# Optimization experiments

Hardware: AMD Instinct MI355X
Metric: run time of the kernel (lower is better)

Reference implementation:

```python
import jax, jax.numpy as jnp
import numpy as np
from jax.scipy.special import logsumexp

B, S, V, H, T = 64, 2048, 32000, 128, 4


def setup_inputs() -> dict:
    key = jax.random.key(0)
    ks = jax.random.split(key, 14)
    s = 0.02
    inp = {
        'x': jax.random.randint(ks[0], (B, S), 1, V),          # token ids (avoid pad idx 0)
        'y': jax.random.randint(ks[1], (B, S), 0, T),           # gold tags
        'mask': jnp.ones((B, S), dtype=bool),
        'emb': (jax.random.normal(ks[2], (V, H)) * s).at[0].set(0.0),  # padding_idx=0
        'w1': jax.random.normal(ks[3], (H, H, 3)) * 0.05,  # OIH conv kernels
        'b1': jnp.zeros((H,)),
        'w2': jax.random.normal(ks[4], (H, H, 3)) * 0.05,
        'b2': jnp.zeros((H,)),
        'w3': jax.random.normal(ks[5], (H, H, 3)) * 0.05,
        'b3': jnp.zeros((H,)),
        'dw': jax.random.normal(ks[6], (H, T)) * s,
        'db': jnp.zeros((T,)),
        'start_t': jax.random.normal(ks[7], (T,)) * 0.1,
        'end_t': jax.random.normal(ks[8], (T,)) * 0.1,
        'trans': jax.random.normal(ks[9], (T, T)) * 0.1,
    }
    return inp


def _conv_relu(h, w, b):
    # h: [B, C, S]; replicate (edge) padding of 1 on sequence axis, kernel 3, stride 1
    hp = jnp.pad(h, ((0, 0), (0, 0), (1, 1)), mode='edge')
    o = jax.lax.conv_general_dilated(hp, w, (1,), 'VALID',
                                     dimension_numbers=('NCH', 'OIH', 'NCH'))
    return jax.nn.relu(o + b[None, :, None])


def _crf_llh(emissions, tags, mask, start_t, end_t, trans):
    # emissions: [B,S,T], tags: [B,S] int, mask: [B,S] bool. torchcrf sum log-likelihood.
    maskf = mask.astype(emissions.dtype)
    bidx = jnp.arange(emissions.shape[0])
    # numerator: score of gold path
    emit = jnp.take_along_axis(emissions, tags[..., None], axis=2)[..., 0]  # [B,S]
    num = start_t[tags[:, 0]] + emit[:, 0]
    tr = trans[tags[:, :-1], tags[:, 1:]]                                    # [B,S-1]
    num = num + ((tr + emit[:, 1:]) * maskf[:, 1:]).sum(axis=1)
    lengths = maskf.sum(axis=1).astype(jnp.int32)
    num = num + end_t[tags[bidx, lengths - 1]]
    # denominator: forward algorithm (sequential logsumexp DP over tags)
    alpha0 = start_t[None, :] + emissions[:, 0]                               # [B,T]
    def step(alpha, xs):
        e_t, m_t = xs                                                         # [B,T], [B]
        nxt = logsumexp(alpha[:, :, None] + trans[None], axis=1) + e_t
        return jnp.where(m_t[:, None], nxt, alpha), None
    alpha, _ = jax.lax.scan(step, alpha0,
                            (emissions[:, 1:].transpose(1, 0, 2), mask[:, 1:].T))
    den = logsumexp(alpha + end_t[None, :], axis=1)                           # [B]
    return (num - den).sum()


def reference(x, y, mask, emb, w1, b1, w2, b2, w3, b3, dw, db, start_t, end_t, trans):
    h = emb[x]                           # [B,S,H]
    h = h.transpose(0, 2, 1)             # [B,H,S] for conv channels
    h = _conv_relu(h, w1, b1)
    h = _conv_relu(h, w2, b2)
    h = _conv_relu(h, w3, b3)
    h = h.transpose(0, 2, 1)             # [B,S,H]
    emissions = jnp.einsum('bsh,ht->bst', h, dw) + db
    return _crf_llh(emissions, y, mask, start_t, end_t, trans)
```

## Files before the change

### kernel.cpp

```cpp
#include <hip/hip_runtime.h>

#define BB 64
#define SS 2048
#define VV 32000
#define HH 128
#define TT 4
#define NSLOT 96
#define CHST (NSLOT*16)
#define BUFSZ (8*CHST)
#define SCL 0x7F7F7F7F

typedef long long i64;
using f32x16 = __attribute__((ext_vector_type(16))) float;
using i32x8  = __attribute__((ext_vector_type(8))) int;

typedef const __attribute__((address_space(1))) unsigned int* gas_ptr;
typedef __attribute__((address_space(3))) unsigned int* las_ptr;

__device__ __forceinline__ unsigned pk4_fp8(float a, float b, float c, float d) {
  unsigned r = __builtin_amdgcn_cvt_pk_fp8_f32(a, b, 0, false);
  r = __builtin_amdgcn_cvt_pk_fp8_f32(c, d, r, true);
  return r;
}
__device__ __forceinline__ unsigned char f2fp8(float v) {
  return (unsigned char)(__builtin_amdgcn_cvt_pk_fp8_f32(v, 0.f, 0, false) & 0xff);
}

__device__ __forceinline__ i32x8 load_af(const char* base) {
  union { i32x8 v; uint4 q[2]; } u;
  u.q[0] = *reinterpret_cast<const uint4*>(base);
  u.q[1] = *reinterpret_cast<const uint4*>(base + CHST);
  return u.v;
}

__global__ __launch_bounds__(256) void pack_kernel(
    const float* __restrict__ w1, const float* __restrict__ w2,
    const float* __restrict__ w3, const float* __restrict__ dw,
    const float* __restrict__ emb,
    unsigned char* __restrict__ wQ8, unsigned char* __restrict__ dwMF,
    unsigned char* __restrict__ emb8)
{
  int idx = blockIdx.x * 256 + threadIdx.x;
  if (idx < 147456) {
    int f = idx >> 11;
    int r = idx & 2047;
    int lane = r >> 5, q = r & 31;
    int kb = f % 6;
    int t2 = f / 6;
    int oq = t2 & 3, layer = t2 >> 2;
    int o = oq * 32 + (lane & 31);
    int k = kb * 64 + (lane >> 5) * 32 + q;
    int tap = k >> 7, i = k & 127;
    const float* w = layer == 0 ? w1 : (layer == 1 ? w2 : w3);
    wQ8[idx] = f2fp8(w[(o * HH + i) * 3 + tap] * 16.f);
  } else if (idx < 151552) {
    int idx2 = idx - 147456;
    int kb = idx2 >> 9;
    int r = idx2 & 511;
    int lane = r >> 3, j = r & 7;
    int row = lane & 31;
    int ch = kb * 16 + (lane >> 5) * 8 + j;
    dwMF[idx2] = (row < 4) ? f2fp8(dw[ch * TT + row] * 16.f) : 0;
  } else {
    int e = idx - 151552;
    if (e < VV * HH / 8) {
      const float* src = emb + (size_t)e * 8;
      float4 f0 = *reinterpret_cast<const float4*>(src);
      float4 f1 = *reinterpret_cast<const float4*>(src + 4);
      uint2 v;
      v.x = pk4_fp8(f0.x * 16.f, f0.y * 16.f, f0.z * 16.f, f0.w * 16.f);
      v.y = pk4_fp8(f1.x * 16.f, f1.y * 16.f, f1.z * 16.f, f1.w * 16.f);
      *reinterpret_cast<uint2*>(emb8 + (size_t)e * 8) = v;
    }
  }
}

__global__ __launch_bounds__(256, 3) void conv_fused(
    const unsigned char* __restrict__ emb8, const int* __restrict__ x,
    const unsigned char* __restrict__ wQ8,
    const float* __restrict__ b1, const float* __restrict__ b2,
    const float* __restrict__ b3,
    const unsigned char* __restrict__ dwMF, const float* __restrict__ db,
    float* __restrict__ emis)
{
  __shared__ char smem[BUFSZ];

  const int blk  = blockIdx.x;
  const int bb   = blk >> 5;
  const int p0   = (blk & 31) << 6;
  const int tid  = threadIdx.x;
  const int lane = tid & 63;
  const int wv   = tid >> 6;
  const int l31  = lane & 31;
  const int lh   = lane >> 5;
  const int oq   = wv;
  const int lhc  = lh * 2 * CHST;

  int swA[3][3], swC[2][3];
#pragma unroll
  for (int pf = 0; pf < 3; pf++)
#pragma unroll
    for (int tap = 0; tap < 3; tap++) {
      int pos = p0 - 16 + pf * 32 + l31 + tap - 1;
      pos = pos < 0 ? 0 : (pos > SS - 1 ? SS - 1 : pos);
      int r = pos - p0 + 16;
      r = r < 0 ? 0 : (r > NSLOT - 1 ? NSLOT - 1 : r);
      swA[pf][tap] = r * 16;
    }
#pragma unroll
  for (int pf = 0; pf < 2; pf++)
#pragma unroll
    for (int tap = 0; tap < 3; tap++) {
      int pos = p0 + pf * 32 + l31 + tap - 1;
      pos = pos < 0 ? 0 : (pos > SS - 1 ? SS - 1 : pos);
      int r = pos - p0 + 16;
      r = r < 0 ? 0 : (r > NSLOT - 1 ? NSLOT - 1 : r);
      swC[pf][tap] = r * 16;
    }

  const unsigned char* wq0 = wQ8 + (size_t)oq * 12288;

  i32x8 wfa = *reinterpret_cast<const i32x8*>(wq0 + lane * 32);
  i32x8 wfb = *reinterpret_cast<const i32x8*>(wq0 + 2048 + lane * 32);

  int tokA, tokB;
  {
    int sA = p0 - 16 + lane;
    sA = sA < 0 ? 0 : (sA > SS - 1 ? SS - 1 : sA);
    tokA = x[bb * SS + sA];
    int sB = p0 + 16 + lane;
    sB = sB < 0 ? 0 : (sB > SS - 1 ? SS - 1 : sB);
    tokB = x[bb * SS + sB];
  }
#pragma unroll
  for (int ci = 0; ci < 2; ci++) {
    int c = wv * 2 + ci;
    const unsigned char* srcA = emb8 + (size_t)tokA * HH + c * 16;
    const unsigned char* srcB = emb8 + (size_t)tokB * HH + c * 16;
    __builtin_amdgcn_global_load_lds((gas_ptr)(const void*)srcA,
                                     (las_ptr)(void*)(smem + c * CHST), 16, 0, 0);
    __builtin_amdgcn_global_load_lds((gas_ptr)(const void*)srcB,
                                     (las_ptr)(void*)(smem + c * CHST + 32 * 16), 16, 0, 0);
  }

#pragma unroll 1
  for (int layer = 0; layer < 2; layer++) {
    const unsigned char* wqb  = wq0 + layer * 49152;
    const unsigned char* wqbn = wqb + 49152;
    const float* bias = (layer == 0) ? b1 : b2;

    i32x8 wf[6];
    wf[0] = wfa; wf[1] = wfb;

    if (layer == 0) {
      asm volatile("s_waitcnt vmcnt(0)" ::: "memory");
      __syncthreads();
    }

    f32x16 acc[3];
#pragma unroll
    for (int pf = 0; pf < 3; pf++)
#pragma unroll
      for (int i = 0; i < 16; i++) acc[pf][i] = 0.f;

    i32x8 afc[3];
#pragma unroll
    for (int pf = 0; pf < 3; pf++)
      afc[pf] = load_af(smem + lhc + swA[pf][0]);

#pragma unroll
    for (int kb = 0; kb < 6; kb++) {
      if (kb < 4) {
        wf[kb + 2] = *reinterpret_cast<const i32x8*>(wqb + (kb + 2) * 2048 + lane * 32);
      } else {
        i32x8 v = *reinterpret_cast<const i32x8*>(wqbn + (kb - 4) * 2048 + lane * 32);
        if (kb == 4) wfa = v; else wfb = v;
      }
      const int kn = kb + 1;
      const int cbn = ((kn & 1) * 4) * CHST + lhc;
      const int tapn = kn >> 1;
#pragma unroll
      for (int pf = 0; pf < 3; pf++) {
        i32x8 nxt;
        if (kb < 5)
          nxt = load_af(smem + cbn + swA[pf][tapn]);
        acc[pf] = __builtin_amdgcn_mfma_scale_f32_32x32x64_f8f6f4(
            wf[kb], afc[pf], acc[pf], 0, 0, 0, SCL, 0, SCL);
        if (kb < 5) afc[pf] = nxt;
      }
    }

    __syncthreads();

    float4 b16[4];
#pragma unroll
    for (int g = 0; g < 4; g++) {
      float4 bv = *reinterpret_cast<const float4*>(bias + oq * 32 + g * 8 + lh * 4);
      b16[g].x = bv.x * 16.f; b16[g].y = bv.y * 16.f;
      b16[g].z = bv.z * 16.f; b16[g].w = bv.w * 16.f;
    }
#pragma unroll
    for (int pf = 0; pf < 3; pf++) {
      int slot = pf * 32 + l31;
#pragma unroll
      for (int g = 0; g < 4; g++) {
        float v0 = fmaxf(fmaf(acc[pf][4 * g + 0], 0.0625f, b16[g].x), 0.f);
        float v1 = fmaxf(fmaf(acc[pf][4 * g + 1], 0.0625f, b16[g].y), 0.f);
        float v2 = fmaxf(fmaf(acc[pf][4 * g + 2], 0.0625f, b16[g].z), 0.f);
        float v3 = fmaxf(fmaf(acc[pf][4 * g + 3], 0.0625f, b16[g].w), 0.f);
        unsigned pk = pk4_fp8(v0, v1, v2, v3);
        *reinterpret_cast<unsigned*>(
            smem + (oq * 2 + (g >> 1)) * CHST + slot * 16 + (g & 1) * 8 + lh * 4) = pk;
      }
    }
    __syncthreads();
  }

  {
    const unsigned char* wqb = wq0 + 2 * 49152;
    i32x8 wf[6];
    wf[0] = wfa; wf[1] = wfb;

    f32x16 acc[2];
#pragma unroll
    for (int pf = 0; pf < 2; pf++)
#pragma unroll
      for (int i = 0; i < 16; i++) acc[pf][i] = 0.f;

    i32x8 afc[2];
#pragma unroll
    for (int pf = 0; pf < 2; pf++)
      afc[pf] = load_af(smem + lhc + swC[pf][0]);

#pragma unroll
    for (int kb = 0; kb < 6; kb++) {
      if (kb < 4)
        wf[kb + 2] = *reinterpret_cast<const i32x8*>(wqb + (kb + 2) * 2048 + lane * 32);
      const int kn = kb + 1;
      const int cbn = ((kn & 1) * 4) * CHST + lhc;
      const int tapn = kn >> 1;
#pragma unroll
      for (int pf = 0; pf < 2; pf++) {
        i32x8 nxt;
        if (kb < 5)
          nxt = load_af(smem + cbn + swC[pf][tapn]);
        acc[pf] = __builtin_amdgcn_mfma_scale_f32_32x32x64_f8f6f4(
            wf[kb], afc[pf], acc[pf], 0, 0, 0, SCL, 0, SCL);
        if (kb < 5) afc[pf] = nxt;
      }
    }

    __syncthreads();

    float4 b16[4];
#pragma unroll
    for (int g = 0; g < 4; g++) {
      float4 bv = *reinterpret_cast<const float4*>(b3 + oq * 32 + g * 8 + lh * 4);
      b16[g].x = bv.x * 16.f; b16[g].y = bv.y * 16.f;
      b16[g].z = bv.z * 16.f; b16[g].w = bv.w * 16.f;
    }
#pragma unroll
    for (int pf = 0; pf < 2; pf++) {
      int slot = 16 + pf * 32 + l31;
#pragma unroll
      for (int g = 0; g < 4; g++) {
        float v0 = fmaxf(fmaf(acc[pf][4 * g + 0], 0.0625f, b16[g].x), 0.f);
        float v1 = fmaxf(fmaf(acc[pf][4 * g + 1], 0.0625f, b16[g].y), 0.f);
        float v2 = fmaxf(fmaf(acc[pf][4 * g + 2], 0.0625f, b16[g].z), 0.f);
        float v3 = fmaxf(fmaf(acc[pf][4 * g + 3], 0.0625f, b16[g].w), 0.f);
        unsigned pk = pk4_fp8(v0, v1, v2, v3);
        *reinterpret_cast<unsigned*>(
            smem + (oq * 2 + (g >> 1)) * CHST + slot * 16 + (g & 1) * 8 + lh * 4) = pk;
      }
    }
    __syncthreads();
  }

  if (wv < 2) {
    float4 dbv = *reinterpret_cast<const float4*>(db);
    f32x16 e;
#pragma unroll
    for (int i = 0; i < 16; i++) e[i] = 0.f;
    const int slot = 16 + wv * 32 + l31;
#pragma unroll
    for (int kb = 0; kb < 8; kb++) {
      i64 a = *reinterpret_cast<const i64*>(dwMF + kb * 512 + lane * 8);
      i64 h = *reinterpret_cast<const i64*>(smem + kb * CHST + slot * 16 + lh * 8);
      e = __builtin_amdgcn_mfma_f32_32x32x16_fp8_fp8(a, h, e, 0, 0, 0);
    }
    if (lane < 32) {
      float4 o;
      o.x = e[0] * (1.f / 256.f) + dbv.x;
      o.y = e[1] * (1.f / 256.f) + dbv.y;
      o.z = e[2] * (1.f / 256.f) + dbv.z;
      o.w = e[3] * (1.f / 256.f) + dbv.w;
      *reinterpret_cast<float4*>(emis + ((size_t)(bb * SS + p0 + wv * 32 + l31)) * TT) = o;
    }
  }
}

__global__ __launch_bounds__(256) void crf_stage1(
    const float* __restrict__ emis, const int* __restrict__ y,
    const float* __restrict__ start_t, const float* __restrict__ end_t,
    const float* __restrict__ trans, float* __restrict__ num_out,
    float* __restrict__ Mout)
{
  int blk = blockIdx.x;
  int tid = threadIdx.x;
  if (blk < 64) {
    int b = blk;
    float sum = 0.f;
    for (int s = tid; s < SS; s += 256) {
      int yc = y[b * SS + s];
      float v = emis[((size_t)b * SS + s) * TT + yc];
      if (s > 0) v += trans[y[b * SS + s - 1] * TT + yc];
      sum += v;
    }
    __shared__ float red[256];
    red[tid] = sum;
    __syncthreads();
    for (int off = 128; off > 0; off >>= 1) {
      if (tid < off) red[tid] += red[tid + off];
      __syncthreads();
    }
    if (tid == 0)
      num_out[b] = red[0] + start_t[y[b * SS]] + end_t[y[b * SS + SS - 1]];
    return;
  }
  int gi = (blk - 64) * 256 + tid;
  int g = gi >> 2;
  int i = gi & 3;
  int b = g >> 6, c = g & 63;
  float tr[16];
#pragma unroll
  for (int t = 0; t < 16; t++) tr[t] = trans[t];
  float m0 = (i == 0) ? 0.f : -1e30f;
  float m1 = (i == 1) ? 0.f : -1e30f;
  float m2 = (i == 2) ? 0.f : -1e30f;
  float m3 = (i == 3) ? 0.f : -1e30f;
  int slo = 1 + c * 32;
  int shi = slo + 32; if (shi > SS) shi = SS;
  for (int s = slo; s < shi; s++) {
    float4 e = *reinterpret_cast<const float4*>(emis + ((size_t)b * SS + s) * TT);
    float n0, n1, n2, n3;
    {
      float t0 = m0 + tr[0], t1 = m1 + tr[4], t2 = m2 + tr[8], t3 = m3 + tr[12];
      float mx = fmaxf(fmaxf(t0, t1), fmaxf(t2, t3));
      n0 = e.x + mx + __logf(__expf(t0-mx) + __expf(t1-mx) + __expf(t2-mx) + __expf(t3-mx));
    }
    {
      float t0 = m0 + tr[1], t1 = m1 + tr[5], t2 = m2 + tr[9], t3 = m3 + tr[13];
      float mx = fmaxf(fmaxf(t0, t1), fmaxf(t2, t3));
      n1 = e.y + mx + __logf(__expf(t0-mx) + __expf(t1-mx) + __expf(t2-mx) + __expf(t3-mx));
    }
    {
      float t0 = m0 + tr[2], t1 = m1 + tr[6], t2 = m2 + tr[10], t3 = m3 + tr[14];
      float mx = fmaxf(fmaxf(t0, t1), fmaxf(t2, t3));
      n2 = e.z + mx + __logf(__expf(t0-mx) + __expf(t1-mx) + __expf(t2-mx) + __expf(t3-mx));
    }
    {
      float t0 = m0 + tr[3], t1 = m1 + tr[7], t2 = m2 + tr[11], t3 = m3 + tr[15];
      float mx = fmaxf(fmaxf(t0, t1), fmaxf(t2, t3));
      n3 = e.w + mx + __logf(__expf(t0-mx) + __expf(t1-mx) + __expf(t2-mx) + __expf(t3-mx));
    }
    m0 = n0; m1 = n1; m2 = n2; m3 = n3;
  }
  float4 outv = {m0, m1, m2, m3};
  *reinterpret_cast<float4*>(Mout + (size_t)g * 16 + i * 4) = outv;
}

__global__ __launch_bounds__(256) void final_kernel(
    const float* __restrict__ emis, const float* __restrict__ Mchunks,
    const float* __restrict__ num, const float* __restrict__ start_t,
    const float* __restrict__ end_t, float* __restrict__ out)
{
  int tid = threadIdx.x;
  int b = tid >> 2, j = tid & 3;
  int lane = tid & 63, qb = lane & ~3;
  float a = start_t[j] + emis[((size_t)b * SS) * TT + j];
  for (int c = 0; c < 64; c++) {
    const float* M = Mchunks + ((size_t)b * 64 + c) * 16;
    float a0 = __shfl(a, qb + 0, 64);
    float a1 = __shfl(a, qb + 1, 64);
    float a2 = __shfl(a, qb + 2, 64);
    float a3 = __shfl(a, qb + 3, 64);
    float t0 = a0 + M[0*4 + j];
    float t1 = a1 + M[1*4 + j];
    float t2 = a2 + M[2*4 + j];
    float t3 = a3 + M[3*4 + j];
    float mx = fmaxf(fmaxf(t0, t1), fmaxf(t2, t3));
    a = mx + __logf(__expf(t0-mx) + __expf(t1-mx) + __expf(t2-mx) + __expf(t3-mx));
  }
  a += end_t[j];
  float a0 = __shfl(a, qb + 0, 64);
  float a1 = __shfl(a, qb + 1, 64);
  float a2 = __shfl(a, qb + 2, 64);
  float a3 = __shfl(a, qb + 3, 64);
  float mx = fmaxf(fmaxf(a0, a1), fmaxf(a2, a3));
  float den = mx + __logf(__expf(a0-mx) + __expf(a1-mx) + __expf(a2-mx) + __expf(a3-mx));
  float r = num[b] - den;
  __shared__ float red[64];
  if (j == 0) red[b] = r;
  __syncthreads();
  if (tid < 64) {
    float v = red[tid];
#pragma unroll
    for (int off = 32; off > 0; off >>= 1) v += __shfl_down(v, off);
    if (tid == 0) out[0] = v;
  }
}

extern "C" void kernel_launch(void* const* d_in, const int* in_sizes, int n_in,
                              void* d_out, int out_size, void* d_ws, size_t ws_size,
                              hipStream_t stream)
{
  const int*   x     = (const int*)  d_in[0];
  const int*   y     = (const int*)  d_in[1];
  const float* emb   = (const float*)d_in[3];
  const float* w1    = (const float*)d_in[4];
  const float* b1    = (const float*)d_in[5];
  const float* w2    = (const float*)d_in[6];
  const float* b2    = (const float*)d_in[7];
  const float* w3    = (const float*)d_in[8];
  const float* b3    = (const float*)d_in[9];
  const float* dw    = (const float*)d_in[10];
  const float* db    = (const float*)d_in[11];
  const float* start = (const float*)d_in[12];
  const float* endt  = (const float*)d_in[13];
  const float* trans = (const float*)d_in[14];

  char* ws = (char*)d_ws;
  const size_t WQ8_OFF  = 0;
  const size_t DWMF_OFF = 147456;
  const size_t NUM_OFF  = 151552;
  const size_t CHM_OFF  = 151808;
  const size_t EMIS_OFF = 413952;
  const size_t EMB8_OFF = 2511104;

  unsigned char* wQ8p  = (unsigned char*)(ws + WQ8_OFF);
  unsigned char* dwMFp = (unsigned char*)(ws + DWMF_OFF);
  float*         numb  = (float*)(ws + NUM_OFF);
  float*         chM   = (float*)(ws + CHM_OFF);
  float*         emis  = (float*)(ws + EMIS_OFF);
  unsigned char* emb8p = (unsigned char*)(ws + EMB8_OFF);

  hipLaunchKernelGGL(pack_kernel, dim3(2592), dim3(256), 0, stream,
                     w1, w2, w3, dw, emb, wQ8p, dwMFp, emb8p);

  hipLaunchKernelGGL(conv_fused, dim3(BB * 32), dim3(256), 0, stream,
                     emb8p, x, wQ8p, b1, b2, b3, dwMFp, db, emis);

  hipLaunchKernelGGL(crf_stage1, dim3(128), dim3(256), 0, stream,
                     emis, y, start, endt, trans, numb, chM);
  hipLaunchKernelGGL(final_kernel, dim3(1), dim3(256), 0, stream,
                     emis, chM, numb, start, endt, (float*)d_out);
}
```

Baseline: 71.61 us.

## Fuse CRF numerator and chunked forward pass into conv kernel epilogue

The separate crf_stage1 kernel is removed. Each conv block now keeps its 64 emission rows in shared memory and uses two wavefronts to compute the gold-path partial score and the 4x4 chunk transfer matrix (log-semiring) for its 64-position chunk. This removes the round trip of the full emissions array through global memory and one kernel launch. In exchange the conv kernel gains a serial 64-step tail on one wave per block and a little extra LDS, which could affect occupancy. The final kernel now combines 32 chunks per sequence and sums the per-block numerator partials.

```diff
diff --git a/kernel.cpp b/kernel.cpp
--- a/kernel.cpp
+++ b/kernel.cpp
@@ -77,17 +77,22 @@
 
 __global__ __launch_bounds__(256, 3) void conv_fused(
     const unsigned char* __restrict__ emb8, const int* __restrict__ x,
+    const int* __restrict__ y,
     const unsigned char* __restrict__ wQ8,
     const float* __restrict__ b1, const float* __restrict__ b2,
     const float* __restrict__ b3,
     const unsigned char* __restrict__ dwMF, const float* __restrict__ db,
-    float* __restrict__ emis)
+    const float* __restrict__ start_t, const float* __restrict__ end_t,
+    const float* __restrict__ trans,
+    float* __restrict__ emis0, float* __restrict__ num_part,
+    float* __restrict__ chM)
 {
-  __shared__ char smem[BUFSZ];
+  __shared__ char smem[BUFSZ + 1024];
 
   const int blk  = blockIdx.x;
   const int bb   = blk >> 5;
-  const int p0   = (blk & 31) << 6;
+  const int q    = blk & 31;
+  const int p0   = q << 6;
   const int tid  = threadIdx.x;
   const int lane = tid & 63;
   const int wv   = tid >> 6;
@@ -95,6 +100,7 @@
   const int lh   = lane >> 5;
   const int oq   = wv;
   const int lhc  = lh * 2 * CHST;
+  float4* emisL  = reinterpret_cast<float4*>(smem + BUFSZ);
 
   int swA[3][3], swC[2][3];
 #pragma unroll
@@ -294,100 +300,89 @@
       o.y = e[1] * (1.f / 256.f) + dbv.y;
       o.z = e[2] * (1.f / 256.f) + dbv.z;
       o.w = e[3] * (1.f / 256.f) + dbv.w;
-      *reinterpret_cast<float4*>(emis + ((size_t)(bb * SS + p0 + wv * 32 + l31)) * TT) = o;
-    }
-  }
-}
-
-__global__ __launch_bounds__(256) void crf_stage1(
-    const float* __restrict__ emis, const int* __restrict__ y,
-    const float* __restrict__ start_t, const float* __restrict__ end_t,
-    const float* __restrict__ trans, float* __restrict__ num_out,
-    float* __restrict__ Mout)
-{
-  int blk = blockIdx.x;
-  int tid = threadIdx.x;
-  if (blk < 64) {
-    int b = blk;
-    float sum = 0.f;
-    for (int s = tid; s < SS; s += 256) {
-      int yc = y[b * SS + s];
-      float v = emis[((size_t)b * SS + s) * TT + yc];
-      if (s > 0) v += trans[y[b * SS + s - 1] * TT + yc];
-      sum += v;
-    }
-    __shared__ float red[256];
-    red[tid] = sum;
-    __syncthreads();
-    for (int off = 128; off > 0; off >>= 1) {
-      if (tid < off) red[tid] += red[tid + off];
-      __syncthreads();
-    }
-    if (tid == 0)
-      num_out[b] = red[0] + start_t[y[b * SS]] + end_t[y[b * SS + SS - 1]];
-    return;
-  }
-  int gi = (blk - 64) * 256 + tid;
-  int g = gi >> 2;
-  int i = gi & 3;
-  int b = g >> 6, c = g & 63;
-  float tr[16];
-#pragma unroll
-  for (int t = 0; t < 16; t++) tr[t] = trans[t];
-  float m0 = (i == 0) ? 0.f : -1e30f;
-  float m1 = (i == 1) ? 0.f : -1e30f;
-  float m2 = (i == 2) ? 0.f : -1e30f;
-  float m3 = (i == 3) ? 0.f : -1e30f;
-  int slo = 1 + c * 32;
-  int shi = slo + 32; if (shi > SS) shi = SS;
-  for (int s = slo; s < shi; s++) {
-    float4 e = *reinterpret_cast<const float4*>(emis + ((size_t)b * SS + s) * TT);
-    float n0, n1, n2, n3;
-    {
-      float t0 = m0 + tr[0], t1 = m1 + tr[4], t2 = m2 + tr[8], t3 = m3 + tr[12];
-      float mx = fmaxf(fmaxf(t0, t1), fmaxf(t2, t3));
-      n0 = e.x + mx + __logf(__expf(t0-mx) + __expf(t1-mx) + __expf(t2-mx) + __expf(t3-mx));
-    }
-    {
-      float t0 = m0 + tr[1], t1 = m1 + tr[5], t2 = m2 + tr[9], t3 = m3 + tr[13];
-      float mx = fmaxf(fmaxf(t0, t1), fmaxf(t2, t3));
-      n1 = e.y + mx + __logf(__expf(t0-mx) + __expf(t1-mx) + __expf(t2-mx) + __expf(t3-mx));
-    }
-    {
-      float t0 = m0 + tr[2], t1 = m1 + tr[6], t2 = m2 + tr[10], t3 = m3 + tr[14];
-      float mx = fmaxf(fmaxf(t0, t1), fmaxf(t2, t3));
-      n2 = e.z + mx + __logf(__expf(t0-mx) + __expf(t1-mx) + __expf(t2-mx) + __expf(t3-mx));
-    }
-    {
-      float t0 = m0 + tr[3], t1 = m1 + tr[7], t2 = m2 + tr[11], t3 = m3 + tr[15];
-      float mx = fmaxf(fmaxf(t0, t1), fmaxf(t2, t3));
-      n3 = e.w + mx + __logf(__expf(t0-mx) + __expf(t1-mx) + __expf(t2-mx) + __expf(t3-mx));
-    }
-    m0 = n0; m1 = n1; m2 = n2; m3 = n3;
-  }
-  float4 outv = {m0, m1, m2, m3};
-  *reinterpret_cast<float4*>(Mout + (size_t)g * 16 + i * 4) = outv;
+      emisL[wv * 32 + l31] = o;
+      if (q == 0 && tid == 0)
+        *reinterpret_cast<float4*>(emis0 + bb * 4) = o;
+    }
+  }
+  __syncthreads();
+
+  if (wv == 2) {
+    int s = p0 + lane;
+    int yc = y[bb * SS + s];
+    float4 e4 = emisL[lane];
+    float v = (yc == 0) ? e4.x : (yc == 1) ? e4.y : (yc == 2) ? e4.z : e4.w;
+    if (s > 0) {
+      int yp = y[bb * SS + s - 1];
+      v += trans[yp * TT + yc];
+    }
+    if (q == 0 && lane == 0) v += start_t[yc];
+    if (q == 31 && lane == 63) v += end_t[yc];
+#pragma unroll
+    for (int off = 32; off > 0; off >>= 1) v += __shfl_down(v, off);
+    if (lane == 0) num_part[blk] = v;
+  }
+
+  if (wv == 3 && lane < 4) {
+    float tr[16];
+#pragma unroll
+    for (int t = 0; t < 4; t++) {
+      float4 t4 = *reinterpret_cast<const float4*>(trans + t * 4);
+      tr[t * 4 + 0] = t4.x; tr[t * 4 + 1] = t4.y;
+      tr[t * 4 + 2] = t4.z; tr[t * 4 + 3] = t4.w;
+    }
+    float m0 = (lane == 0) ? 0.f : -1e30f;
+    float m1 = (lane == 1) ? 0.f : -1e30f;
+    float m2 = (lane == 2) ? 0.f : -1e30f;
+    float m3 = (lane == 3) ? 0.f : -1e30f;
+    for (int s = (q == 0) ? 1 : 0; s < 64; s++) {
+      float4 e = emisL[s];
+      float n0, n1, n2, n3;
+      {
+        float t0 = m0 + tr[0], t1 = m1 + tr[4], t2 = m2 + tr[8], t3 = m3 + tr[12];
+        float mx = fmaxf(fmaxf(t0, t1), fmaxf(t2, t3));
+        n0 = e.x + mx + __logf(__expf(t0-mx) + __expf(t1-mx) + __expf(t2-mx) + __expf(t3-mx));
+      }
+      {
+        float t0 = m0 + tr[1], t1 = m1 + tr[5], t2 = m2 + tr[9], t3 = m3 + tr[13];
+        float mx = fmaxf(fmaxf(t0, t1), fmaxf(t2, t3));
+        n1 = e.y + mx + __logf(__expf(t0-mx) + __expf(t1-mx) + __expf(t2-mx) + __expf(t3-mx));
+      }
+      {
+        float t0 = m0 + tr[2], t1 = m1 + tr[6], t2 = m2 + tr[10], t3 = m3 + tr[14];
+        float mx = fmaxf(fmaxf(t0, t1), fmaxf(t2, t3));
+        n2 = e.z + mx + __logf(__expf(t0-mx) + __expf(t1-mx) + __expf(t2-mx) + __expf(t3-mx));
+      }
+      {
+        float t0 = m0 + tr[3], t1 = m1 + tr[7], t2 = m2 + tr[11], t3 = m3 + tr[15];
+        float mx = fmaxf(fmaxf(t0, t1), fmaxf(t2, t3));
+        n3 = e.w + mx + __logf(__expf(t0-mx) + __expf(t1-mx) + __expf(t2-mx) + __expf(t3-mx));
+      }
+      m0 = n0; m1 = n1; m2 = n2; m3 = n3;
+    }
+    float4 outv = {m0, m1, m2, m3};
+    *reinterpret_cast<float4*>(chM + (size_t)blk * 16 + lane * 4) = outv;
+  }
 }
 
 __global__ __launch_bounds__(256) void final_kernel(
-    const float* __restrict__ emis, const float* __restrict__ Mchunks,
-    const float* __restrict__ num, const float* __restrict__ start_t,
+    const float* __restrict__ emis0, const float* __restrict__ chM,
+    const float* __restrict__ num_part, const float* __restrict__ start_t,
     const float* __restrict__ end_t, float* __restrict__ out)
 {
   int tid = threadIdx.x;
   int b = tid >> 2, j = tid & 3;
   int lane = tid & 63, qb = lane & ~3;
-  float a = start_t[j] + emis[((size_t)b * SS) * TT + j];
-  for (int c = 0; c < 64; c++) {
-    const float* M = Mchunks + ((size_t)b * 64 + c) * 16;
+  float a = start_t[j] + emis0[b * 4 + j];
+  const float* Mb = chM + (size_t)b * 512;
+  for (int c = 0; c < 32; c++) {
+    const float* M = Mb + c * 16;
+    float m0 = M[0 * 4 + j], m1 = M[1 * 4 + j], m2 = M[2 * 4 + j], m3 = M[3 * 4 + j];
     float a0 = __shfl(a, qb + 0, 64);
     float a1 = __shfl(a, qb + 1, 64);
     float a2 = __shfl(a, qb + 2, 64);
     float a3 = __shfl(a, qb + 3, 64);
-    float t0 = a0 + M[0*4 + j];
-    float t1 = a1 + M[1*4 + j];
-    float t2 = a2 + M[2*4 + j];
-    float t3 = a3 + M[3*4 + j];
+    float t0 = a0 + m0, t1 = a1 + m1, t2 = a2 + m2, t3 = a3 + m3;
     float mx = fmaxf(fmaxf(t0, t1), fmaxf(t2, t3));
     a = mx + __logf(__expf(t0-mx) + __expf(t1-mx) + __expf(t2-mx) + __expf(t3-mx));
   }
@@ -398,7 +393,13 @@
   float a3 = __shfl(a, qb + 3, 64);
   float mx = fmaxf(fmaxf(a0, a1), fmaxf(a2, a3));
   float den = mx + __logf(__expf(a0-mx) + __expf(a1-mx) + __expf(a2-mx) + __expf(a3-mx));
-  float r = num[b] - den;
+  float ns = 0.f;
+  const float* np = num_part + b * 32 + j * 8;
+#pragma unroll
+  for (int k = 0; k < 8; k++) ns += np[k];
+  ns += __shfl_xor(ns, 1, 64);
+  ns += __shfl_xor(ns, 2, 64);
+  float r = ns - den;
   __shared__ float red[64];
   if (j == 0) red[b] = r;
   __syncthreads();
@@ -432,26 +433,25 @@
   char* ws = (char*)d_ws;
   const size_t WQ8_OFF  = 0;
   const size_t DWMF_OFF = 147456;
-  const size_t NUM_OFF  = 151552;
-  const size_t CHM_OFF  = 151808;
-  const size_t EMIS_OFF = 413952;
-  const size_t EMB8_OFF = 2511104;
+  const size_t EMIS0_OFF= 151552;
+  const size_t NUMP_OFF = 152576;
+  const size_t CHM_OFF  = 160768;
+  const size_t EMB8_OFF = 291840;
 
   unsigned char* wQ8p  = (unsigned char*)(ws + WQ8_OFF);
   unsigned char* dwMFp = (unsigned char*)(ws + DWMF_OFF);
-  float*         numb  = (float*)(ws + NUM_OFF);
+  float*         emis0 = (float*)(ws + EMIS0_OFF);
+  float*         nump  = (float*)(ws + NUMP_OFF);
   float*         chM   = (float*)(ws + CHM_OFF);
-  float*         emis  = (float*)(ws + EMIS_OFF);
   unsigned char* emb8p = (unsigned char*)(ws + EMB8_OFF);
 
   hipLaunchKernelGGL(pack_kernel, dim3(2592), dim3(256), 0, stream,
                      w1, w2, w3, dw, emb, wQ8p, dwMFp, emb8p);
 
   hipLaunchKernelGGL(conv_fused, dim3(BB * 32), dim3(256), 0, stream,
-                     emb8p, x, wQ8p, b1, b2, b3, dwMFp, db, emis);
-
-  hipLaunchKernelGGL(crf_stage1, dim3(128), dim3(256), 0, stream,
-                     emis, y, start, endt, trans, numb, chM);
+                     emb8p, x, y, wQ8p, b1, b2, b3, dwMFp, db,
+                     start, endt, trans, emis0, nump, chM);
+
   hipLaunchKernelGGL(final_kernel, dim3(1), dim3(256), 0, stream,
-                     emis, chM, numb, start, endt, (float*)d_out);
-}
+                     emis0, chM, nump, start, endt, (float*)d_out);
+}
```

After: 121.7 us. 1.7x slower.
